# Kernel optimization log

Hardware: AMD Instinct MI355X
Metric: run time of the kernel (lower is better)

## Reference

```python
import jax, jax.numpy as jnp
import numpy as np

N = 2_000_000      # total active voxels across the batch (post sparse-conv stack)
C = 128            # channels out of the last SparseConv3d block
B = 256            # batch_size
NUM_CLASSES = 4


def _linear_params(key, fan_in, fan_out):
    kw, kb = jax.random.split(key)
    bound = 1.0 / np.sqrt(fan_in)
    W = jax.random.uniform(kw, (fan_in, fan_out), jnp.float32, -bound, bound)
    b = jax.random.uniform(kb, (fan_out,), jnp.float32, -bound, bound)
    return W, b


def setup_inputs() -> dict:
    key = jax.random.key(0)
    ks = jax.random.split(key, 6)
    features = jax.random.normal(ks[0], (N, C), dtype=jnp.float32)
    batch_ids = jnp.sort(jax.random.randint(ks[1], (N,), 0, B, dtype=jnp.int32))
    W1, b1 = _linear_params(ks[2], 2 * C, 128)
    W2, b2 = _linear_params(ks[3], 128, 64)
    W3, b3 = _linear_params(ks[4], 64, 32)
    W4, b4 = _linear_params(ks[5], 32, NUM_CLASSES)
    return {
        "features": features, "batch_ids": batch_ids, "batch_size": B,
        "W1": W1, "b1": b1, "W2": W2, "b2": b2,
        "W3": W3, "b3": b3, "W4": W4, "b4": b4,
    }


def reference(features, batch_ids, batch_size, W1, b1, W2, b2, W3, b3, W4, b4):
    # Fused segment mean+max pooling (replaces the per-batch Python loop).
    seg_sum = jax.ops.segment_sum(features, batch_ids, num_segments=batch_size,
                                  indices_are_sorted=True)            # [B, C]
    counts = jax.ops.segment_sum(jnp.ones((features.shape[0],), features.dtype),
                                 batch_ids, num_segments=batch_size,
                                 indices_are_sorted=True)             # [B]
    seg_max = jax.ops.segment_max(features, batch_ids, num_segments=batch_size,
                                  indices_are_sorted=True)            # [B, C]
    nonempty = (counts > 0)[:, None]
    seg_mean = jnp.where(nonempty, seg_sum / jnp.maximum(counts, 1.0)[:, None], 0.0)
    seg_max = jnp.where(nonempty, seg_max, 0.0)  # empty segments -> zeros (as in torch code)
    pooled = jnp.concatenate([seg_mean, seg_max], axis=1)             # [B, 2C]
    # fc head (Dropout is identity in eval mode)
    h = jax.nn.relu(pooled @ W1 + b1)
    h = jax.nn.relu(h @ W2 + b2)
    h = jax.nn.relu(h @ W3 + b3)
    return h @ W4 + b4                                                # [B, num_classes]
```

## Files before the change

kernel.cpp:

```cpp
#include <hip/hip_runtime.h>

#define CC 128
#define C4V 32

__device__ __forceinline__ unsigned fkey(float f) {
    unsigned b = __float_as_uint(f);
    return (b & 0x80000000u) ? ~b : (b | 0x80000000u);
}
__device__ __forceinline__ float fdec(unsigned k) {
    unsigned b = (k & 0x80000000u) ? (k & 0x7FFFFFFFu) : ~k;
    return __uint_as_float(b);
}

__device__ __forceinline__ void flush_seg(int seg, int c4, const float4& sum, const float4& mx,
                                          int cnt, float* __restrict__ seg_sum,
                                          unsigned* __restrict__ seg_maxk, int* __restrict__ seg_cnt) {
    float* sp = seg_sum + (size_t)seg * CC + c4 * 4;
    atomicAdd(sp + 0, sum.x);
    atomicAdd(sp + 1, sum.y);
    atomicAdd(sp + 2, sum.z);
    atomicAdd(sp + 3, sum.w);
    unsigned* mp = seg_maxk + (size_t)seg * CC + c4 * 4;
    atomicMax(mp + 0, fkey(mx.x));
    atomicMax(mp + 1, fkey(mx.y));
    atomicMax(mp + 2, fkey(mx.z));
    atomicMax(mp + 3, fkey(mx.w));
    if (c4 == 0) atomicAdd(&seg_cnt[seg], cnt);
}

__global__ void __launch_bounds__(256) pool_kernel(
    const float* __restrict__ feats, const int* __restrict__ ids, int N,
    float* __restrict__ seg_sum, unsigned* __restrict__ seg_maxk,
    int* __restrict__ seg_cnt, int rows_per_block)
{
    const int c4 = threadIdx.x & 31;
    const int rl = threadIdx.x >> 5;
    long long r0 = (long long)blockIdx.x * rows_per_block;
    long long r1 = r0 + rows_per_block;
    if (r1 > N) r1 = N;

    float4 sum = make_float4(0.f, 0.f, 0.f, 0.f);
    float4 mx  = make_float4(-3.4e38f, -3.4e38f, -3.4e38f, -3.4e38f);
    int cur = -1, cnt = 0;

    const float4* f4 = (const float4*)feats;
    for (long long r = r0 + rl; r < r1; r += 8) {
        int id = ids[r];
        float4 v = f4[r * C4V + c4];
        if (id != cur) {
            if (cur >= 0)
                flush_seg(cur, c4, sum, mx, cnt, seg_sum, seg_maxk, seg_cnt);
            cur = id;
            sum = make_float4(0.f, 0.f, 0.f, 0.f);
            mx  = make_float4(-3.4e38f, -3.4e38f, -3.4e38f, -3.4e38f);
            cnt = 0;
        }
        sum.x += v.x; sum.y += v.y; sum.z += v.z; sum.w += v.w;
        mx.x = fmaxf(mx.x, v.x); mx.y = fmaxf(mx.y, v.y);
        mx.z = fmaxf(mx.z, v.z); mx.w = fmaxf(mx.w, v.w);
        cnt++;
    }
    if (cur >= 0)
        flush_seg(cur, c4, sum, mx, cnt, seg_sum, seg_maxk, seg_cnt);
}

__global__ void __launch_bounds__(128) head_kernel(
    const float* __restrict__ seg_sum, const unsigned* __restrict__ seg_maxk,
    const int* __restrict__ seg_cnt,
    const float* __restrict__ W1, const float* __restrict__ b1,
    const float* __restrict__ W2, const float* __restrict__ b2,
    const float* __restrict__ W3, const float* __restrict__ b3,
    const float* __restrict__ W4, const float* __restrict__ b4,
    float* __restrict__ out)
{
    __shared__ float pooled[2 * CC];
    __shared__ float h1s[128];
    __shared__ float h2s[64];
    __shared__ float h3s[32];

    const int b = blockIdx.x;
    const int t = threadIdx.x;

    const int cnt = seg_cnt[b];
    const float inv = (cnt > 0) ? (1.f / (float)cnt) : 0.f;

    {
        float s = seg_sum[(size_t)b * CC + t];
        unsigned k = seg_maxk[(size_t)b * CC + t];
        pooled[t] = s * inv;
        pooled[CC + t] = (cnt > 0) ? fdec(k) : 0.f;
    }
    __syncthreads();

    {
        float acc = b1[t];
        for (int i = 0; i < 2 * CC; i++) acc += pooled[i] * W1[i * 128 + t];
        h1s[t] = fmaxf(acc, 0.f);
    }
    __syncthreads();

    if (t < 64) {
        float acc = b2[t];
        for (int i = 0; i < 128; i++) acc += h1s[i] * W2[i * 64 + t];
        h2s[t] = fmaxf(acc, 0.f);
    }
    __syncthreads();

    if (t < 32) {
        float acc = b3[t];
        for (int i = 0; i < 64; i++) acc += h2s[i] * W3[i * 32 + t];
        h3s[t] = fmaxf(acc, 0.f);
    }
    __syncthreads();

    if (t < 4) {
        float acc = b4[t];
        for (int i = 0; i < 32; i++) acc += h3s[i] * W4[i * 4 + t];
        out[b * 4 + t] = acc;
    }
}

extern "C" void kernel_launch(void* const* d_in, const int* in_sizes, int n_in,
                              void* d_out, int out_size, void* d_ws, size_t ws_size,
                              hipStream_t stream) {
    const float* feats = (const float*)d_in[0];
    const int*   ids   = (const int*)d_in[1];
    const float* W1 = (const float*)d_in[3];
    const float* b1 = (const float*)d_in[4];
    const float* W2 = (const float*)d_in[5];
    const float* b2 = (const float*)d_in[6];
    const float* W3 = (const float*)d_in[7];
    const float* b3 = (const float*)d_in[8];
    const float* W4 = (const float*)d_in[9];
    const float* b4 = (const float*)d_in[10];
    float* out = (float*)d_out;

    const int N = in_sizes[1];
    const int NCLS = in_sizes[10];
    const int B = out_size / NCLS;

    float*    seg_sum  = (float*)d_ws;
    unsigned* seg_maxk = (unsigned*)(seg_sum + (size_t)B * CC);
    int*      seg_cnt  = (int*)(seg_maxk + (size_t)B * CC);
    const size_t init_bytes = (size_t)B * CC * 4 * 2 + (size_t)B * 4;
    hipMemsetAsync(d_ws, 0, init_bytes, stream);

    const int rows_per_block = 2048;
    const int grid = (N + rows_per_block - 1) / rows_per_block;
    pool_kernel<<<grid, 256, 0, stream>>>(feats, ids, N, seg_sum, seg_maxk, seg_cnt,
                                          rows_per_block);
    head_kernel<<<B, 128, 0, stream>>>(seg_sum, seg_maxk, seg_cnt,
                                       W1, b1, W2, b2, W3, b3, W4, b4, out);
}
```

Before: 1.328 ms.

## Unroll pooling loop with batched nontemporal loads and shared-memory segment ids

```diff
diff --git a/kernel.cpp b/kernel.cpp
--- a/kernel.cpp
+++ b/kernel.cpp
@@ -2,6 +2,14 @@
 
 #define CC 128
 #define C4V 32
+#define RPB 1024
+#define UNR 8
+
+typedef float f4v __attribute__((ext_vector_type(4)));
+
+__device__ __forceinline__ f4v vsplat(float x) {
+    f4v r; r.x = x; r.y = x; r.z = x; r.w = x; return r;
+}
 
 __device__ __forceinline__ unsigned fkey(float f) {
     unsigned b = __float_as_uint(f);
@@ -12,7 +20,7 @@
     return __uint_as_float(b);
 }
 
-__device__ __forceinline__ void flush_seg(int seg, int c4, const float4& sum, const float4& mx,
+__device__ __forceinline__ void flush_seg(int seg, int c4, const f4v& sum, const f4v& mx,
                                           int cnt, float* __restrict__ seg_sum,
                                           unsigned* __restrict__ seg_maxk, int* __restrict__ seg_cnt) {
     float* sp = seg_sum + (size_t)seg * CC + c4 * 4;
@@ -31,34 +39,87 @@
 __global__ void __launch_bounds__(256) pool_kernel(
     const float* __restrict__ feats, const int* __restrict__ ids, int N,
     float* __restrict__ seg_sum, unsigned* __restrict__ seg_maxk,
-    int* __restrict__ seg_cnt, int rows_per_block)
+    int* __restrict__ seg_cnt)
 {
+    __shared__ int sids[RPB];
+
     const int c4 = threadIdx.x & 31;
     const int rl = threadIdx.x >> 5;
-    long long r0 = (long long)blockIdx.x * rows_per_block;
-    long long r1 = r0 + rows_per_block;
-    if (r1 > N) r1 = N;
-
-    float4 sum = make_float4(0.f, 0.f, 0.f, 0.f);
-    float4 mx  = make_float4(-3.4e38f, -3.4e38f, -3.4e38f, -3.4e38f);
+    const long long r0 = (long long)blockIdx.x * RPB;
+    const int nrows = (r0 + RPB <= N) ? RPB : (int)(N - r0);
+
+    for (int i = threadIdx.x; i < nrows; i += 256)
+        sids[i] = ids[r0 + i];
+    __syncthreads();
+
+    f4v sum = vsplat(0.f);
+    f4v mx  = vsplat(-3.4e38f);
     int cur = -1, cnt = 0;
 
-    const float4* f4 = (const float4*)feats;
-    for (long long r = r0 + rl; r < r1; r += 8) {
-        int id = ids[r];
-        float4 v = f4[r * C4V + c4];
-        if (id != cur) {
-            if (cur >= 0)
-                flush_seg(cur, c4, sum, mx, cnt, seg_sum, seg_maxk, seg_cnt);
-            cur = id;
-            sum = make_float4(0.f, 0.f, 0.f, 0.f);
-            mx  = make_float4(-3.4e38f, -3.4e38f, -3.4e38f, -3.4e38f);
-            cnt = 0;
+    const f4v* __restrict__ fp = (const f4v*)feats + ((long long)r0 + rl) * C4V + c4;
+
+    if (nrows == RPB) {
+        #pragma unroll 1
+        for (int it = 0; it < RPB / (8 * UNR); ++it) {
+            const int lb = it * (8 * UNR) + rl;
+
+            f4v v[UNR];
+            #pragma unroll
+            for (int k = 0; k < UNR; ++k)
+                v[k] = __builtin_nontemporal_load(fp + (size_t)(it * (8 * UNR) + 8 * k) * C4V);
+
+            int idv[UNR];
+            #pragma unroll
+            for (int k = 0; k < UNR; ++k)
+                idv[k] = sids[lb + 8 * k];
+
+            bool same = true;
+            #pragma unroll
+            for (int k = 0; k < UNR; ++k) same &= (idv[k] == cur);
+
+            if (same) {
+                #pragma unroll
+                for (int k = 0; k < UNR; ++k) {
+                    sum.x += v[k].x; sum.y += v[k].y; sum.z += v[k].z; sum.w += v[k].w;
+                    mx.x = fmaxf(mx.x, v[k].x); mx.y = fmaxf(mx.y, v[k].y);
+                    mx.z = fmaxf(mx.z, v[k].z); mx.w = fmaxf(mx.w, v[k].w);
+                }
+                cnt += UNR;
+            } else {
+                #pragma unroll
+                for (int k = 0; k < UNR; ++k) {
+                    if (idv[k] != cur) {
+                        if (cur >= 0)
+                            flush_seg(cur, c4, sum, mx, cnt, seg_sum, seg_maxk, seg_cnt);
+                        cur = idv[k];
+                        sum = vsplat(0.f);
+                        mx  = vsplat(-3.4e38f);
+                        cnt = 0;
+                    }
+                    sum.x += v[k].x; sum.y += v[k].y; sum.z += v[k].z; sum.w += v[k].w;
+                    mx.x = fmaxf(mx.x, v[k].x); mx.y = fmaxf(mx.y, v[k].y);
+                    mx.z = fmaxf(mx.z, v[k].z); mx.w = fmaxf(mx.w, v[k].w);
+                    cnt++;
+                }
+            }
         }
-        sum.x += v.x; sum.y += v.y; sum.z += v.z; sum.w += v.w;
-        mx.x = fmaxf(mx.x, v.x); mx.y = fmaxf(mx.y, v.y);
-        mx.z = fmaxf(mx.z, v.z); mx.w = fmaxf(mx.w, v.w);
-        cnt++;
+    } else {
+        for (int lr = rl; lr < nrows; lr += 8) {
+            int id = sids[lr];
+            f4v v = fp[(size_t)(lr - rl) * C4V];
+            if (id != cur) {
+                if (cur >= 0)
+                    flush_seg(cur, c4, sum, mx, cnt, seg_sum, seg_maxk, seg_cnt);
+                cur = id;
+                sum = vsplat(0.f);
+                mx  = vsplat(-3.4e38f);
+                cnt = 0;
+            }
+            sum.x += v.x; sum.y += v.y; sum.z += v.z; sum.w += v.w;
+            mx.x = fmaxf(mx.x, v.x); mx.y = fmaxf(mx.y, v.y);
+            mx.z = fmaxf(mx.z, v.z); mx.w = fmaxf(mx.w, v.w);
+            cnt++;
+        }
     }
     if (cur >= 0)
         flush_seg(cur, c4, sum, mx, cnt, seg_sum, seg_maxk, seg_cnt);
@@ -145,10 +206,8 @@
     const size_t init_bytes = (size_t)B * CC * 4 * 2 + (size_t)B * 4;
     hipMemsetAsync(d_ws, 0, init_bytes, stream);
 
-    const int rows_per_block = 2048;
-    const int grid = (N + rows_per_block - 1) / rows_per_block;
-    pool_kernel<<<grid, 256, 0, stream>>>(feats, ids, N, seg_sum, seg_maxk, seg_cnt,
-                                          rows_per_block);
+    const int grid = (N + RPB - 1) / RPB;
+    pool_kernel<<<grid, 256, 0, stream>>>(feats, ids, N, seg_sum, seg_maxk, seg_cnt);
     head_kernel<<<B, 128, 0, stream>>>(seg_sum, seg_maxk, seg_cnt,
                                        W1, b1, W2, b2, W3, b3, W4, b4, out);
 }
```

After: 1.285 ms. 1.03x faster.
